# Performance work log

Measured on AMD Instinct MI355X. Metric: run time of the kernel, lower is better.

The kernel has to match this reference:

```python
import jax, jax.numpy as jnp
import numpy as np

K = 3  # spatial window (window_size = [1,3,3,1])


def _extract_patches(x, k):
    """TF-style extract_patches, VALID padding, stride 1, rate 1.
    x: [B,H,W,C] -> [B,Ho,Wo,k*k*C] with depth ordering (ki, kj, c)."""
    B, H, W, C = x.shape
    Ho, Wo = H - k + 1, W - k + 1
    cols = [x[:, ki:ki + Ho, kj:kj + Wo, :] for ki in range(k) for kj in range(k)]
    return jnp.concatenate(cols, axis=-1)


def setup_inputs() -> dict:
    key = jax.random.key(0)
    k1, k2 = jax.random.split(key)
    x = jax.random.normal(k1, (8, 32, 32, 32), dtype=jnp.float32)
    # weight shape per build(): (1, 1, 1, K*K*C, filters) = (1,1,1,288,64)
    w = jax.random.normal(k2, (1, 1, 1, 3 * 3 * 32, 64), dtype=jnp.float32) * 0.05
    bias = jnp.zeros((64,), dtype=jnp.float32)
    return {"x": x, "w": w, "bias": bias}


def reference(x, w, bias):
    # patches: [B,Ho,Wo,KKC]
    p = _extract_patches(x, K)
    # broadcast add: [B,Ho,Wo,KKC,1] + [KKC,F] -> [B,Ho,Wo,KKC,F]
    r = p[..., None] + w[0, 0, 0]
    # tropical conv: max-plus minus min-plus over the patch axis, plus bias
    return jnp.max(r, axis=3) - jnp.min(r, axis=3) + bias
```

## Files before the change

### kernel.cpp

```cpp
#include <hip/hip_runtime.h>
#include <math.h>


typedef _Float16 half2v __attribute__((ext_vector_type(2)));
typedef _Float16 half4v __attribute__((ext_vector_type(4)));

#define WSTRIDE 296

__device__ __forceinline__ void tap(half2v a, half2v& mx, half2v& mn) {
  mx = __builtin_elementwise_max(mx, a);
  mn = __builtin_elementwise_min(mn, a);
}

__global__ __launch_bounds__(512) void trop_kernel(
    const float* __restrict__ x, const float* __restrict__ w,
    const float* __restrict__ bias, float* __restrict__ out) {
  __shared__ _Float16 wt[64 * WSTRIDE];
  __shared__ _Float16 xh[3 * 32 * 32];

  const int i = blockIdx.x;
  const int b = blockIdx.y;
  const int tid = threadIdx.x;
  const int f = tid & 63;
  const int j0 = __builtin_amdgcn_readfirstlane(tid >> 6) * 4;

  const int skq = tid >> 6;
#pragma unroll
  for (int it = 0; it < 9; ++it) {
    int k0 = (it * 8 + skq) * 4;
    const float* wp = w + (size_t)k0 * 64 + f;
    half4v hv;
    hv.x = (_Float16)wp[0 * 64];
    hv.y = (_Float16)wp[1 * 64];
    hv.z = (_Float16)wp[2 * 64];
    hv.w = (_Float16)wp[3 * 64];
    *(half4v*)&wt[f * WSTRIDE + k0] = hv;
  }

  const float* xb = x + (((size_t)b * 32 + i) * 32) * 32;
#pragma unroll
  for (int t = 0; t < 3; ++t) {
    int g = tid + t * 512;
    int ki = g >> 9;
    int rem = g & 511;
    int col = rem >> 4;
    int cp = rem & 15;
    float2 v = *(const float2*)(xb + ki * 1024 + col * 32 + cp * 2);
    half2v h;
    h.x = (_Float16)v.x;
    h.y = (_Float16)v.y;
    *(half2v*)&xh[(ki * 32 + col) * 32 + cp * 2] = h;
  }

  __syncthreads();

  const int cc0 = ((j0 + 0 < 32) ? j0 + 0 : 31) * 32;
  const int cc1 = ((j0 + 1 < 32) ? j0 + 1 : 31) * 32;
  const int cc2 = ((j0 + 2 < 32) ? j0 + 2 : 31) * 32;
  const int cc3 = ((j0 + 3 < 32) ? j0 + 3 : 31) * 32;
  const int cc4 = ((j0 + 4 < 32) ? j0 + 4 : 31) * 32;
  const int cc5 = ((j0 + 5 < 32) ? j0 + 5 : 31) * 32;

  const _Float16 NI = (_Float16)(-INFINITY), PI = (_Float16)INFINITY;
  half2v mx0 = {NI, NI}, mx1 = {NI, NI}, mx2 = {NI, NI}, mx3 = {NI, NI};
  half2v mn0 = {PI, PI}, mn1 = {PI, PI}, mn2 = {PI, PI}, mn3 = {PI, PI};

#pragma clang loop unroll(disable)
  for (int kc = 0; kc < 12; ++kc) {
    const int ki = kc >> 2;
    const int c8 = (kc & 3) << 3;
    const _Float16* xrow = &xh[ki * 1024 + c8];
    const _Float16* wrow = &wt[f * WSTRIDE + ki * 96 + c8];

    uint4 xa0 = *(const uint4*)&xrow[cc0];
    uint4 xa1 = *(const uint4*)&xrow[cc1];
    uint4 xa2 = *(const uint4*)&xrow[cc2];
    uint4 xa3 = *(const uint4*)&xrow[cc3];
    uint4 xa4 = *(const uint4*)&xrow[cc4];
    uint4 xa5 = *(const uint4*)&xrow[cc5];
    uint4 wa0 = *(const uint4*)&wrow[0];
    uint4 wa1 = *(const uint4*)&wrow[32];
    uint4 wa2 = *(const uint4*)&wrow[64];

#define DOD(D)                                                       \
  {                                                                  \
    half2v w0 = __builtin_bit_cast(half2v, wa0.D);                   \
    half2v w1 = __builtin_bit_cast(half2v, wa1.D);                   \
    half2v w2 = __builtin_bit_cast(half2v, wa2.D);                   \
    half2v x0 = __builtin_bit_cast(half2v, xa0.D);                   \
    half2v x1 = __builtin_bit_cast(half2v, xa1.D);                   \
    half2v x2 = __builtin_bit_cast(half2v, xa2.D);                   \
    half2v x3 = __builtin_bit_cast(half2v, xa3.D);                   \
    half2v x4 = __builtin_bit_cast(half2v, xa4.D);                   \
    half2v x5 = __builtin_bit_cast(half2v, xa5.D);                   \
    tap(x0 + w0, mx0, mn0); tap(x1 + w0, mx1, mn1);                  \
    tap(x2 + w0, mx2, mn2); tap(x3 + w0, mx3, mn3);                  \
    tap(x1 + w1, mx0, mn0); tap(x2 + w1, mx1, mn1);                  \
    tap(x3 + w1, mx2, mn2); tap(x4 + w1, mx3, mn3);                  \
    tap(x2 + w2, mx0, mn0); tap(x3 + w2, mx1, mn1);                  \
    tap(x4 + w2, mx2, mn2); tap(x5 + w2, mx3, mn3);                  \
  }
    DOD(x) DOD(y) DOD(z) DOD(w)
#undef DOD
  }

  float bv = bias[f];
  float* ob = out + (((size_t)b * 30 + i) * 30 + j0) * 64 + f;
  if (j0 + 0 < 30) ob[0 * 64] = fmaxf((float)mx0.x, (float)mx0.y) - fminf((float)mn0.x, (float)mn0.y) + bv;
  if (j0 + 1 < 30) ob[1 * 64] = fmaxf((float)mx1.x, (float)mx1.y) - fminf((float)mn1.x, (float)mn1.y) + bv;
  if (j0 + 2 < 30) ob[2 * 64] = fmaxf((float)mx2.x, (float)mx2.y) - fminf((float)mn2.x, (float)mn2.y) + bv;
  if (j0 + 3 < 30) ob[3 * 64] = fmaxf((float)mx3.x, (float)mx3.y) - fminf((float)mn3.x, (float)mn3.y) + bv;
}

extern "C" void kernel_launch(void* const* d_in, const int* in_sizes, int n_in,
                              void* d_out, int out_size, void* d_ws, size_t ws_size,
                              hipStream_t stream) {
  const float* x = (const float*)d_in[0];
  const float* w = (const float*)d_in[1];
  const float* bias = (const float*)d_in[2];
  float* out = (float*)d_out;
  dim3 grid(30, 8);
  dim3 block(512);
  hipLaunchKernelGGL(trop_kernel, grid, block, 0, stream, x, w, bias, out);
}
```

Baseline: 66.71 us.

## Split channel reduction across two wave groups with shared-memory combine

Doubles the block to 1024 threads and splits the 32-channel reduction into two halves, one per group of 8 waves. Partial max/min accumulators are combined through a small shared-memory buffer after an extra barrier. The aim is more waves per block, so the latency of the short per-thread loop is better hidden across 240 blocks. The cost is an extra sync, more shared memory, and the weight staging being duplicated across more threads.

```diff
diff --git a/kernel.cpp b/kernel.cpp
--- a/kernel.cpp
+++ b/kernel.cpp
@@ -12,44 +12,59 @@
   mn = __builtin_elementwise_min(mn, a);
 }
 
-__global__ __launch_bounds__(512) void trop_kernel(
+__device__ __forceinline__ half2v h2(unsigned u) {
+  return __builtin_bit_cast(half2v, u);
+}
+__device__ __forceinline__ unsigned u32(half2v h) {
+  return __builtin_bit_cast(unsigned, h);
+}
+
+__global__ __launch_bounds__(1024) void trop_kernel(
     const float* __restrict__ x, const float* __restrict__ w,
     const float* __restrict__ bias, float* __restrict__ out) {
   __shared__ _Float16 wt[64 * WSTRIDE];
   __shared__ _Float16 xh[3 * 32 * 32];
+  __shared__ uint4 red[8][2][64];
 
   const int i = blockIdx.x;
   const int b = blockIdx.y;
   const int tid = threadIdx.x;
   const int f = tid & 63;
-  const int j0 = __builtin_amdgcn_readfirstlane(tid >> 6) * 4;
+  const int W = __builtin_amdgcn_readfirstlane(tid >> 6);
+  const int j0 = (W & 7) * 4;
+  const int chalf = W >> 3;
 
-  const int skq = tid >> 6;
+  const int q = tid >> 6;
 #pragma unroll
-  for (int it = 0; it < 9; ++it) {
-    int k0 = (it * 8 + skq) * 4;
-    const float* wp = w + (size_t)k0 * 64 + f;
-    half4v hv;
-    hv.x = (_Float16)wp[0 * 64];
-    hv.y = (_Float16)wp[1 * 64];
-    hv.z = (_Float16)wp[2 * 64];
-    hv.w = (_Float16)wp[3 * 64];
-    *(half4v*)&wt[f * WSTRIDE + k0] = hv;
+  for (int it = 0; it < 5; ++it) {
+    int qq = q + it * 16;
+    if (qq < 72) {
+      int k0 = qq * 4;
+      const float* wp = w + (size_t)k0 * 64 + f;
+      half4v hv;
+      hv.x = (_Float16)wp[0 * 64];
+      hv.y = (_Float16)wp[1 * 64];
+      hv.z = (_Float16)wp[2 * 64];
+      hv.w = (_Float16)wp[3 * 64];
+      *(half4v*)&wt[f * WSTRIDE + k0] = hv;
+    }
   }
 
   const float* xb = x + (((size_t)b * 32 + i) * 32) * 32;
 #pragma unroll
-  for (int t = 0; t < 3; ++t) {
-    int g = tid + t * 512;
-    int ki = g >> 9;
-    int rem = g & 511;
-    int col = rem >> 4;
-    int cp = rem & 15;
-    float2 v = *(const float2*)(xb + ki * 1024 + col * 32 + cp * 2);
-    half2v h;
-    h.x = (_Float16)v.x;
-    h.y = (_Float16)v.y;
-    *(half2v*)&xh[(ki * 32 + col) * 32 + cp * 2] = h;
+  for (int t = 0; t < 2; ++t) {
+    int g = tid + t * 1024;
+    if (g < 1536) {
+      int ki = g >> 9;
+      int rem = g & 511;
+      int col = rem >> 4;
+      int cp = rem & 15;
+      float2 v = *(const float2*)(xb + ki * 1024 + col * 32 + cp * 2);
+      half2v h;
+      h.x = (_Float16)v.x;
+      h.y = (_Float16)v.y;
+      *(half2v*)&xh[(ki * 32 + col) * 32 + cp * 2] = h;
+    }
   }
 
   __syncthreads();
@@ -66,9 +81,9 @@
   half2v mn0 = {PI, PI}, mn1 = {PI, PI}, mn2 = {PI, PI}, mn3 = {PI, PI};
 
 #pragma clang loop unroll(disable)
-  for (int kc = 0; kc < 12; ++kc) {
-    const int ki = kc >> 2;
-    const int c8 = (kc & 3) << 3;
+  for (int kc = 0; kc < 6; ++kc) {
+    const int ki = kc >> 1;
+    const int c8 = ((kc & 1) << 3) + (chalf << 4);
     const _Float16* xrow = &xh[ki * 1024 + c8];
     const _Float16* wrow = &wt[f * WSTRIDE + ki * 96 + c8];
 
@@ -82,34 +97,55 @@
     uint4 wa1 = *(const uint4*)&wrow[32];
     uint4 wa2 = *(const uint4*)&wrow[64];
 
-#define DOD(D)                                                       \
-  {                                                                  \
-    half2v w0 = __builtin_bit_cast(half2v, wa0.D);                   \
-    half2v w1 = __builtin_bit_cast(half2v, wa1.D);                   \
-    half2v w2 = __builtin_bit_cast(half2v, wa2.D);                   \
-    half2v x0 = __builtin_bit_cast(half2v, xa0.D);                   \
-    half2v x1 = __builtin_bit_cast(half2v, xa1.D);                   \
-    half2v x2 = __builtin_bit_cast(half2v, xa2.D);                   \
-    half2v x3 = __builtin_bit_cast(half2v, xa3.D);                   \
-    half2v x4 = __builtin_bit_cast(half2v, xa4.D);                   \
-    half2v x5 = __builtin_bit_cast(half2v, xa5.D);                   \
-    tap(x0 + w0, mx0, mn0); tap(x1 + w0, mx1, mn1);                  \
-    tap(x2 + w0, mx2, mn2); tap(x3 + w0, mx3, mn3);                  \
-    tap(x1 + w1, mx0, mn0); tap(x2 + w1, mx1, mn1);                  \
-    tap(x3 + w1, mx2, mn2); tap(x4 + w1, mx3, mn3);                  \
-    tap(x2 + w2, mx0, mn0); tap(x3 + w2, mx1, mn1);                  \
-    tap(x4 + w2, mx2, mn2); tap(x5 + w2, mx3, mn3);                  \
+#define DOD(D)                                               \
+  {                                                          \
+    half2v w0 = h2(wa0.D);                                   \
+    half2v w1 = h2(wa1.D);                                   \
+    half2v w2 = h2(wa2.D);                                   \
+    half2v x0 = h2(xa0.D);                                   \
+    half2v x1 = h2(xa1.D);                                   \
+    half2v x2 = h2(xa2.D);                                   \
+    half2v x3 = h2(xa3.D);                                   \
+    half2v x4 = h2(xa4.D);                                   \
+    half2v x5 = h2(xa5.D);                                   \
+    tap(x0 + w0, mx0, mn0); tap(x1 + w0, mx1, mn1);          \
+    tap(x2 + w0, mx2, mn2); tap(x3 + w0, mx3, mn3);          \
+    tap(x1 + w1, mx0, mn0); tap(x2 + w1, mx1, mn1);          \
+    tap(x3 + w1, mx2, mn2); tap(x4 + w1, mx3, mn3);          \
+    tap(x2 + w2, mx0, mn0); tap(x3 + w2, mx1, mn1);          \
+    tap(x4 + w2, mx2, mn2); tap(x5 + w2, mx3, mn3);          \
   }
     DOD(x) DOD(y) DOD(z) DOD(w)
 #undef DOD
   }
 
-  float bv = bias[f];
-  float* ob = out + (((size_t)b * 30 + i) * 30 + j0) * 64 + f;
-  if (j0 + 0 < 30) ob[0 * 64] = fmaxf((float)mx0.x, (float)mx0.y) - fminf((float)mn0.x, (float)mn0.y) + bv;
-  if (j0 + 1 < 30) ob[1 * 64] = fmaxf((float)mx1.x, (float)mx1.y) - fminf((float)mn1.x, (float)mn1.y) + bv;
-  if (j0 + 2 < 30) ob[2 * 64] = fmaxf((float)mx2.x, (float)mx2.y) - fminf((float)mn2.x, (float)mn2.y) + bv;
-  if (j0 + 3 < 30) ob[3 * 64] = fmaxf((float)mx3.x, (float)mx3.y) - fminf((float)mn3.x, (float)mn3.y) + bv;
+  if (W >= 8) {
+    uint4 pm, pn;
+    pm.x = u32(mx0); pm.y = u32(mx1); pm.z = u32(mx2); pm.w = u32(mx3);
+    pn.x = u32(mn0); pn.y = u32(mn1); pn.z = u32(mn2); pn.w = u32(mn3);
+    red[W - 8][0][f] = pm;
+    red[W - 8][1][f] = pn;
+  }
+  __syncthreads();
+  if (W < 8) {
+    uint4 pm = red[W][0][f];
+    uint4 pn = red[W][1][f];
+    mx0 = __builtin_elementwise_max(mx0, h2(pm.x));
+    mx1 = __builtin_elementwise_max(mx1, h2(pm.y));
+    mx2 = __builtin_elementwise_max(mx2, h2(pm.z));
+    mx3 = __builtin_elementwise_max(mx3, h2(pm.w));
+    mn0 = __builtin_elementwise_min(mn0, h2(pn.x));
+    mn1 = __builtin_elementwise_min(mn1, h2(pn.y));
+    mn2 = __builtin_elementwise_min(mn2, h2(pn.z));
+    mn3 = __builtin_elementwise_min(mn3, h2(pn.w));
+
+    float bv = bias[f];
+    float* ob = out + (((size_t)b * 30 + i) * 30 + j0) * 64 + f;
+    if (j0 + 0 < 30) ob[0 * 64] = fmaxf((float)mx0.x, (float)mx0.y) - fminf((float)mn0.x, (float)mn0.y) + bv;
+    if (j0 + 1 < 30) ob[1 * 64] = fmaxf((float)mx1.x, (float)mx1.y) - fminf((float)mn1.x, (float)mn1.y) + bv;
+    if (j0 + 2 < 30) ob[2 * 64] = fmaxf((float)mx2.x, (float)mx2.y) - fminf((float)mn2.x, (float)mn2.y) + bv;
+    if (j0 + 3 < 30) ob[3 * 64] = fmaxf((float)mx3.x, (float)mx3.y) - fminf((float)mn3.x, (float)mn3.y) + bv;
+  }
 }
 
 extern "C" void kernel_launch(void* const* d_in, const int* in_sizes, int n_in,
@@ -120,6 +156,6 @@
   const float* bias = (const float*)d_in[2];
   float* out = (float*)d_out;
   dim3 grid(30, 8);
-  dim3 block(512);
+  dim3 block(1024);
   hipLaunchKernelGGL(trop_kernel, grid, block, 0, stream, x, w, bias, out);
 }
```

Result: no change. 66.62 us (-0.1%).
